# Kernel tuning notes

Measured on AMD Instinct MI355X. Metric: run time of the kernel, lower is better.

Reference implementation:

```python
import jax, jax.numpy as jnp
import numpy as np

NUM_CLS = 80
NUM_CONVS = 4
GROUPS = 32
STRIDES = [8, 16, 32, 64, 128]
SIZES = [32.0, 64.0, 128.0, 256.0, 512.0]
CLS_BIAS_INIT = -float(np.log((1 - 0.01) / 0.01))


def _conv(x, w, b):
    # NCHW 3x3 stride-1 same-pad conv
    y = jax.lax.conv_general_dilated(x, w, (1, 1), 'SAME',
                                     dimension_numbers=('NCHW', 'OIHW', 'NCHW'))
    return y + b[None, :, None, None]


def _group_norm(x, gamma, beta, eps=1e-5):
    B, C, H, W = x.shape
    xr = x.reshape(B, GROUPS, C // GROUPS, H, W)
    m = xr.mean(axis=(2, 3, 4), keepdims=True)
    v = xr.var(axis=(2, 3, 4), keepdims=True)
    xn = ((xr - m) / jnp.sqrt(v + eps)).reshape(B, C, H, W)
    return xn * gamma[None, :, None, None] + beta[None, :, None, None]


def _tower(x, ws, bs, gs, betas):
    # CGR block: Conv -> GroupNorm -> ReLU, repeated NUM_CONVS times
    for i in range(NUM_CONVS):
        x = jax.nn.relu(_group_norm(_conv(x, ws[i], bs[i]), gs[i], betas[i]))
    return x


def _build_anchors(h, w, stride, size):
    half = size / 2.0  # single scale=1, ratio=1 -> one square anchor per cell
    yv, xv = jnp.meshgrid(jnp.arange(h, dtype=jnp.float32),
                          jnp.arange(w, dtype=jnp.float32), indexing='ij')
    grid = jnp.stack([xv, yv, xv, yv], axis=-1)  # [h,w,4]
    delta = jnp.array([-half, -half, half, half], dtype=jnp.float32)
    return ((grid + 0.5) * stride + delta).reshape(-1, 4)  # [h*w,4]


def setup_inputs() -> dict:
    key = jax.random.key(0)
    ks = jax.random.split(key, 16)
    C = 256
    feats = {}
    hw = [80, 40, 20, 10, 5]
    for i, name in enumerate(['p3', 'p4', 'p5', 'p6', 'p7']):
        feats[name] = jax.random.normal(ks[i], (8, C, hw[i], hw[i]), dtype=jnp.float32)
    std = 0.01
    inp = dict(feats)
    # cls tower
    inp['cls_tw'] = jax.random.normal(ks[5], (NUM_CONVS, C, C, 3, 3), jnp.float32) * std
    inp['cls_tb'] = jnp.zeros((NUM_CONVS, C), jnp.float32)
    inp['cls_tg'] = jnp.ones((NUM_CONVS, C), jnp.float32)
    inp['cls_tbeta'] = jnp.zeros((NUM_CONVS, C), jnp.float32)
    # reg tower
    inp['reg_tw'] = jax.random.normal(ks[6], (NUM_CONVS, C, C, 3, 3), jnp.float32) * std
    inp['reg_tb'] = jnp.zeros((NUM_CONVS, C), jnp.float32)
    inp['reg_tg'] = jnp.ones((NUM_CONVS, C), jnp.float32)
    inp['reg_tbeta'] = jnp.zeros((NUM_CONVS, C), jnp.float32)
    # heads (num_anchors = 1)
    inp['cls_hw'] = jax.random.normal(ks[7], (NUM_CLS, C, 3, 3), jnp.float32) * std
    inp['cls_hb'] = jnp.full((NUM_CLS,), CLS_BIAS_INIT, jnp.float32)
    inp['reg_hw'] = jax.random.normal(ks[8], (4, C, 3, 3), jnp.float32) * std
    inp['reg_hb'] = jnp.zeros((4,), jnp.float32)
    inp['iou_hw'] = jax.random.normal(ks[9], (1, C, 3, 3), jnp.float32) * std
    inp['iou_hb'] = jnp.zeros((1,), jnp.float32)
    inp['scales'] = jnp.ones((5,), jnp.float32)
    return inp


def reference(p3, p4, p5, p6, p7,
              cls_tw, cls_tb, cls_tg, cls_tbeta,
              reg_tw, reg_tb, reg_tg, reg_tbeta,
              cls_hw, cls_hb, reg_hw, reg_hb, iou_hw, iou_hb, scales):
    feats = [p3, p4, p5, p6, p7]
    outs = []
    for j, x in enumerate(feats):
        B, _, H, W = x.shape
        ct = _tower(x, cls_tw, cls_tb, cls_tg, cls_tbeta)
        rt = _tower(x, reg_tw, reg_tb, reg_tg, reg_tbeta)
        # heads: permute to NHWC then flatten spatial (num_anchors=1)
        cls = _conv(ct, cls_hw, cls_hb).transpose(0, 2, 3, 1).reshape(B, -1, NUM_CLS)
        reg = _conv(rt, reg_hw, reg_hb).transpose(0, 2, 3, 1).reshape(B, -1, 4) * scales[j]
        iou = _conv(rt, iou_hw, iou_hb).transpose(0, 2, 3, 1).reshape(B, -1, 1)  # on_reg=True
        # decode boxes against anchors
        anchor = _build_anchors(H, W, STRIDES[j], SIZES[j])  # [HW,4]
        awh = anchor[:, 2:] - anchor[:, :2]
        actr = anchor[:, :2] + 0.5 * awh
        xy = reg[..., :2] * awh + actr
        wh = jnp.exp(reg[..., 2:]) * awh
        box = jnp.concatenate([xy - 0.5 * wh, xy + 0.5 * wh], axis=-1)
        outs.append(jnp.concatenate([box, iou, cls], axis=-1))
    return jnp.concatenate(outs, axis=1)  # [B, 8525, 85]
```

## Files before the change

kernel.cpp:

```cpp
#include <hip/hip_runtime.h>
#include <stdint.h>

typedef unsigned short u16;
typedef unsigned int u32;
typedef short short8 __attribute__((ext_vector_type(8)));
typedef float f32x4 __attribute__((ext_vector_type(4)));

#define GN_CHUNK 800
#define GN_MAXCH 8

struct LevelTab {
  int Hf[5], Wf[5], Hp[5], Wp[5], HW[5], M[5], mtcum[5], aoff[5];
  int gch[5];
  long xoffp[5], moff[5], ppcum[5], mcum[5];
  float asize[5], astride[5];
};

__device__ __forceinline__ u16 f2bf(float f) {
  u32 u = __float_as_uint(f);
  u = (u + 0x7fffu + ((u >> 16) & 1u)) >> 16;
  return (u16)u;
}
__device__ __forceinline__ float bflo(u32 v) { return __uint_as_float(v << 16); }
__device__ __forceinline__ float bfhi(u32 v) { return __uint_as_float(v & 0xffff0000u); }

__device__ __forceinline__ void gload16(const void* g, void* l) {
  __builtin_amdgcn_global_load_lds((__attribute__((address_space(1))) void*)(g),
                                   (__attribute__((address_space(3))) void*)(l),
                                   16, 0, 0);
}

__global__ __launch_bounds__(256) void prep_tower_w(const float* __restrict__ cls_tw,
                                                    const float* __restrict__ reg_tw,
                                                    u16* __restrict__ W2t) {
  long t = (long)blockIdx.x * 256 + threadIdx.x;
  const long total = 2L * 4 * 256 * 2304;
  if (t >= total) return;
  int ci = (int)(t & 255);
  long u = t >> 8;
  int j = (int)(u % 9); u /= 9;
  int co = (int)(u & 255); u >>= 8;
  int layer = (int)(u & 3);
  int tw = (int)(u >> 2);
  const float* src = tw ? reg_tw : cls_tw;
  float v = src[(((long)layer * 256 + co) * 256 + ci) * 9 + j];
  W2t[t] = f2bf(v);
}

__global__ __launch_bounds__(256) void prep_cls_w(const float* __restrict__ cls_hw,
                                                  u16* __restrict__ W2c) {
  long t = (long)blockIdx.x * 256 + threadIdx.x;
  if (t >= 128L * 2304) return;
  int ci = (int)(t & 255);
  long u = t >> 8;
  int j = (int)(u % 9);
  int co = (int)(u / 9);
  float v = (co < 80) ? cls_hw[(((long)co * 256 + ci) * 9 + j)] : 0.f;
  W2c[t] = f2bf(v);
}

__global__ __launch_bounds__(256) void prep_reg_w(const float* __restrict__ reg_hw,
                                                  const float* __restrict__ iou_hw,
                                                  u16* __restrict__ W2r) {
  long t = (long)blockIdx.x * 256 + threadIdx.x;
  if (t >= 5L * 2304) return;
  int ci = (int)(t & 255);
  long u = t >> 8;
  int j = (int)(u % 9);
  int o = (int)(u / 9);
  float v = (o < 4) ? reg_hw[(((long)o * 256 + ci) * 9 + j)] : iou_hw[(long)ci * 9 + j];
  W2r[t] = f2bf(v);
}

__global__ __launch_bounds__(256) void convert_in(const float* __restrict__ i0, const float* __restrict__ i1,
                                                  const float* __restrict__ i2, const float* __restrict__ i3,
                                                  const float* __restrict__ i4, u16* __restrict__ X0,
                                                  LevelTab lt) {
  long t = (long)blockIdx.x * 256 + threadIdx.x;
  if (t >= lt.ppcum[4] * 32) return;
  const int c8 = (int)(t & 31);
  long pp = t >> 5;
  int lvl = 0;
#pragma unroll
  for (int i = 0; i < 4; ++i) lvl += (pp >= lt.ppcum[i]);
  const long lp = pp - (lvl ? lt.ppcum[lvl - 1] : 0);
  const int Hp = lt.Hp[lvl], Wp = lt.Wp[lvl], Wf = lt.Wf[lvl], HW = lt.HW[lvl];
  const int HpWp = Hp * Wp;
  const int n = (int)(lp / HpWp);
  const int rem = (int)(lp - (long)n * HpWp);
  const int yp = rem / Wp, xp = rem - yp * Wp;
  u16* op = X0 + (lt.xoffp[lvl] + lp) * 256 + c8 * 8;
  if (yp == 0 || yp == Hp - 1 || xp == 0 || xp == Wp - 1) {
    *(uint4*)op = make_uint4(0u, 0u, 0u, 0u);
    return;
  }
  const float* src = lvl == 0 ? i0 : lvl == 1 ? i1 : lvl == 2 ? i2 : lvl == 3 ? i3 : i4;
  const int y = yp - 1, x = xp - 1;
  const long sb = ((long)n * 256 + c8 * 8) * HW + (long)y * Wf + x;
  u32 o4[4];
#pragma unroll
  for (int i = 0; i < 4; ++i) {
    float f0 = src[sb + (long)(2 * i) * HW];
    float f1 = src[sb + (long)(2 * i + 1) * HW];
    o4[i] = (u32)f2bf(f0) | ((u32)f2bf(f1) << 16);
  }
  *(uint4*)op = make_uint4(o4[0], o4[1], o4[2], o4[3]);
}

template <int MODE>
__global__ __launch_bounds__(256, 2) void conv_mfma(
    const u16* __restrict__ XpadA, const u16* __restrict__ XpadB,
    const u16* __restrict__ W2A, const u16* __restrict__ W2B,
    const float* __restrict__ biasA, const float* __restrict__ biasB,
    u16* __restrict__ OtmpA, u16* __restrict__ OtmpB,
    float* __restrict__ Oout, int NP, LevelTab lt) {
  __shared__ __align__(16) u16 sA[3][128 * 32];
  __shared__ __align__(16) u16 sB[3][128 * 32];

  const int nwg = gridDim.x;
  const int qq = nwg >> 3, rr = nwg & 7;
  const int xcd = blockIdx.x & 7, ib = blockIdx.x >> 3;
  const int sid = (xcd < rr ? xcd * (qq + 1) : rr * (qq + 1) + (xcd - rr) * qq) + ib;

  int path, tileId, nt;
  if (MODE == 0) {
    if (NP == 2) {
      const int half = nwg >> 1;
      path = (sid >= half) ? 1 : 0;
      const int inner = sid - path * half;
      tileId = inner >> 1;
      nt = inner & 1;
    } else {
      path = 0;
      tileId = sid >> 1;
      nt = sid & 1;
    }
  } else {
    path = 0;
    tileId = sid;
    nt = 0;
  }
  const u16* __restrict__ Xpad = path ? XpadB : XpadA;
  const u16* __restrict__ W2 = path ? W2B : W2A;
  const float* __restrict__ bias = path ? biasB : biasA;
  u16* __restrict__ Otmp = path ? OtmpB : OtmpA;

  int lvl = 0;
#pragma unroll
  for (int i = 0; i < 4; ++i) lvl += (tileId >= lt.mtcum[i]);
  const int mt = tileId - (lvl ? lt.mtcum[lvl - 1] : 0);
  const int Hp = lt.Hp[lvl], Wp = lt.Wp[lvl], Wf = lt.Wf[lvl];
  const int HW = lt.HW[lvl], M = lt.M[lvl];
  const long xbase = lt.xoffp[lvl] * 256;

  const int tid = threadIdx.x;
  const int w = tid >> 6, lane = tid & 63;
  const int rsub = lane >> 2;
  const int r0 = w * 16 + rsub;
  const int q2 = ((lane & 3) - ((lane >> 3) & 3)) & 3;

  long gA[2], gB[2];
#pragma unroll
  for (int i = 0; i < 2; ++i) {
    int ml = mt * 128 + r0 + i * 64;
    if (ml > M - 1) ml = M - 1;
    const int n = ml / HW;
    const int pr = ml - n * HW;
    const int y = pr / Wf;
    const int x = pr - y * Wf;
    gA[i] = xbase + ((long)((n * Hp + y) * Wp + x)) * 256 + q2 * 8;
    gB[i] = (long)(nt * 128 + r0 + i * 64) * 2304 + q2 * 8;
  }

  const int wm = w >> 1, wn = w & 1;
  const int lm = lane & 15;
  const int slot8 = ((((lane >> 4) + ((lane >> 1) & 3)) & 3) << 3);

  f32x4 acc[4][4];
#pragma unroll
  for (int a = 0; a < 4; ++a)
#pragma unroll
    for (int c = 0; c < 4; ++c) acc[a][c] = {0.f, 0.f, 0.f, 0.f};

  auto STAGE = [&](int kk, int buf) {
    const int j = kk >> 3;
    const int c0 = (kk & 7) << 5;
    const int jy = j / 3, jx = j - jy * 3;
    const long aK = ((long)(jy * Wp + jx)) * 256 + c0;
    const long bK = (long)kk << 5;
    gload16(Xpad + gA[0] + aK, sA[buf] + w * 512);
    gload16(Xpad + gA[1] + aK, sA[buf] + 2048 + w * 512);
    gload16(W2 + gB[0] + bK, sB[buf] + w * 512);
    gload16(W2 + gB[1] + bK, sB[buf] + 2048 + w * 512);
  };

  short8 a0[4], b0[4], a1[4], b1[4];
  auto FRAG0 = [&](int cur) {
    const u16* pa = sA[cur];
    const u16* pb = sB[cur];
#pragma unroll
    for (int mi = 0; mi < 4; ++mi)
      a0[mi] = *(const short8*)(pa + ((wm * 64 + mi * 16 + lm) << 5) + slot8);
#pragma unroll
    for (int ni = 0; ni < 4; ++ni)
      b0[ni] = *(const short8*)(pb + ((wn * 64 + ni * 16 + lm) << 5) + slot8);
  };
  auto FRAG1 = [&](int cur) {
    const u16* pa = sA[cur];
    const u16* pb = sB[cur];
#pragma unroll
    for (int mi = 0; mi < 4; ++mi)
      a1[mi] = *(const short8*)(pa + ((wm * 64 + mi * 16 + lm) << 5) + slot8);
#pragma unroll
    for (int ni = 0; ni < 4; ++ni)
      b1[ni] = *(const short8*)(pb + ((wn * 64 + ni * 16 + lm) << 5) + slot8);
  };
  auto MFMA0 = [&]() {
    __builtin_amdgcn_s_setprio(1);
#pragma unroll
    for (int mi = 0; mi < 4; ++mi)
#pragma unroll
      for (int ni = 0; ni < 4; ++ni)
        acc[mi][ni] = __builtin_amdgcn_mfma_f32_16x16x32_bf16(a0[mi], b0[ni], acc[mi][ni], 0, 0, 0);
    __builtin_amdgcn_s_setprio(0);
  };
  auto MFMA1 = [&]() {
    __builtin_amdgcn_s_setprio(1);
#pragma unroll
    for (int mi = 0; mi < 4; ++mi)
#pragma unroll
      for (int ni = 0; ni < 4; ++ni)
        acc[mi][ni] = __builtin_amdgcn_mfma_f32_16x16x32_bf16(a1[mi], b1[ni], acc[mi][ni], 0, 0, 0);
    __builtin_amdgcn_s_setprio(0);
  };

  STAGE(0, 0);
  STAGE(1, 1);
  asm volatile("s_waitcnt vmcnt(4)" ::: "memory");
  __builtin_amdgcn_s_barrier();
  FRAG0(0);
  STAGE(2, 2);

  int rd = 1;
  int st = 0;
  for (int kk = 0; kk < 68; kk += 2) {
    asm volatile("s_waitcnt vmcnt(4)" ::: "memory");
    __builtin_amdgcn_s_barrier();
    FRAG1(rd);
    rd = rd == 2 ? 0 : rd + 1;
    STAGE(kk + 3, st);
    st = st == 2 ? 0 : st + 1;
    MFMA0();
    asm volatile("s_waitcnt vmcnt(4)" ::: "memory");
    __builtin_amdgcn_s_barrier();
    FRAG0(rd);
    rd = rd == 2 ? 0 : rd + 1;
    STAGE(kk + 4, st);
    st = st == 2 ? 0 : st + 1;
    MFMA1();
  }
  asm volatile("s_waitcnt vmcnt(4)" ::: "memory");
  __builtin_amdgcn_s_barrier();
  FRAG1(rd);
  rd = rd == 2 ? 0 : rd + 1;
  STAGE(71, st);
  MFMA0();
  asm volatile("s_waitcnt vmcnt(4)" ::: "memory");
  __builtin_amdgcn_s_barrier();
  FRAG0(rd);
  rd = rd == 2 ? 0 : rd + 1;
  MFMA1();
  asm volatile("s_waitcnt vmcnt(0)" ::: "memory");
  __builtin_amdgcn_s_barrier();
  FRAG1(rd);
  MFMA0();
  MFMA1();

  const int mwb = mt * 128 + wm * 64;
  const int colb = nt * 128 + wn * 64;
  const int rq4 = (lane >> 4) << 2;
#pragma unroll
  for (int ni = 0; ni < 4; ++ni) {
    const int col = colb + ni * 16 + lm;
    if (MODE == 1 && col >= 80) continue;
    const float bv = bias[col];
#pragma unroll
    for (int mi = 0; mi < 4; ++mi) {
      const int rb = mwb + mi * 16 + rq4;
#pragma unroll
      for (int rg = 0; rg < 4; ++rg) {
        const int ml = rb + rg;
        if (ml < M) {
          const float v = acc[mi][ni][rg] + bv;
          if (MODE == 0) {
            Otmp[(lt.moff[lvl] + ml) * 256 + col] = f2bf(v);
          } else {
            const int nb = ml / HW;
            const int pr = ml - nb * HW;
            Oout[((long)nb * 8525 + lt.aoff[lvl] + pr) * 85 + 5 + col] = v;
          }
        }
      }
    }
  }
}

__global__ __launch_bounds__(256) void gn_part(const u16* __restrict__ tmpA,
                                               const u16* __restrict__ tmpB,
                                               float* __restrict__ part, int perPath,
                                               LevelTab lt) {
  const int bid = blockIdx.x;
  const int path = bid / perPath;
  int r = bid - path * perPath;
  int lvl = 0;
#pragma unroll
  for (int i = 0; i < 4; ++i) {
    const int c = 8 * lt.gch[i];
    if (r >= c) { r -= c; lvl = i + 1; } else break;
  }
  const int b = r / lt.gch[lvl];
  const int chunk = r - b * lt.gch[lvl];
  const u16* __restrict__ tmp = path ? tmpB : tmpA;
  const int HW = lt.HW[lvl];
  const int start = chunk * GN_CHUNK;
  const int end = (start + GN_CHUNK < HW) ? start + GN_CHUNK : HW;

  const int tid = threadIdx.x;
  const int c8 = tid & 31, po = tid >> 5;
  const long base = (lt.moff[lvl] + (long)b * HW) * 256 + c8 * 8;
  float s = 0.f, ss = 0.f;
  for (int p = start + po; p < end; p += 8) {
    const uint4 r4 = *(const uint4*)(tmp + base + (long)p * 256);
    const u32 u[4] = {r4.x, r4.y, r4.z, r4.w};
#pragma unroll
    for (int i = 0; i < 4; ++i) {
      float f0 = bflo(u[i]), f1 = bfhi(u[i]);
      s += f0 + f1;
      ss += f0 * f0 + f1 * f1;
    }
  }
  s += __shfl_down(s, 32);
  ss += __shfl_down(ss, 32);
  __shared__ float rs[4][32], rss[4][32];
  const int w = tid >> 6, lane = tid & 63;
  if (lane < 32) { rs[w][lane] = s; rss[w][lane] = ss; }
  __syncthreads();
  if (tid < 32) {
    const float S = rs[0][tid] + rs[1][tid] + rs[2][tid] + rs[3][tid];
    const float SS = rss[0][tid] + rss[1][tid] + rss[2][tid] + rss[3][tid];
    const long slot = ((long)((path * 1280 + lvl * 256 + b * 32 + tid) * GN_MAXCH + chunk)) * 2;
    part[slot] = S;
    part[slot + 1] = SS;
  }
}

__global__ __launch_bounds__(256) void gn_final(const float* __restrict__ part,
                                                float* __restrict__ stats, LevelTab lt) {
  const int idx = blockIdx.x * 256 + threadIdx.x;
  if (idx >= 2 * 1280) return;
  const int lb = idx % 1280;
  const int lvl = lb >> 8;
  const int nch = lt.gch[lvl];
  float s = 0.f, ss = 0.f;
  const long sbase = (long)idx * GN_MAXCH * 2;
  for (int c = 0; c < nch; ++c) {
    s += part[sbase + c * 2];
    ss += part[sbase + c * 2 + 1];
  }
  const float inv = 1.f / (float)(lt.HW[lvl] * 8);
  const float mean = s * inv;
  const float var = ss * inv - mean * mean;
  stats[idx * 2 + 0] = mean;
  stats[idx * 2 + 1] = rsqrtf(var + 1e-5f);
}

__global__ __launch_bounds__(256) void gn_apply(const u16* __restrict__ tmpA,
                                                const u16* __restrict__ tmpB,
                                                const float* __restrict__ stats,
                                                const float* __restrict__ gammaA,
                                                const float* __restrict__ betaA,
                                                const float* __restrict__ gammaB,
                                                const float* __restrict__ betaB,
                                                u16* __restrict__ poutA, u16* __restrict__ poutB,
                                                int ppBlocks, LevelTab lt) {
  const int path = blockIdx.x / ppBlocks;
  const int xb = blockIdx.x - path * ppBlocks;
  const u16* __restrict__ tmp = path ? tmpB : tmpA;
  const float* __restrict__ gamma = path ? gammaB : gammaA;
  const float* __restrict__ beta = path ? betaB : betaA;
  u16* __restrict__ pout = path ? poutB : poutA;

  long t = (long)xb * 256 + threadIdx.x;
  if (t >= lt.ppcum[4] * 32) return;
  const int c8 = (int)(t & 31);
  long pp = t >> 5;
  int lvl = 0;
#pragma unroll
  for (int i = 0; i < 4; ++i) lvl += (pp >= lt.ppcum[i]);
  const long lp = pp - (lvl ? lt.ppcum[lvl - 1] : 0);
  const int Hp = lt.Hp[lvl], Wp = lt.Wp[lvl], Wf = lt.Wf[lvl], HW = lt.HW[lvl];
  const int HpWp = Hp * Wp;
  const int n = (int)(lp / HpWp);
  const int rem = (int)(lp - (long)n * HpWp);
  const int yp = rem / Wp, xp = rem - yp * Wp;
  u16* op = pout + (lt.xoffp[lvl] + lp) * 256 + c8 * 8;
  if (yp == 0 || yp == Hp - 1 || xp == 0 || xp == Wp - 1) {
    *(uint4*)op = make_uint4(0u, 0u, 0u, 0u);
    return;
  }
  const long m = lt.moff[lvl] + (long)n * HW + (long)(yp - 1) * Wf + (xp - 1);
  const uint4 r = *(const uint4*)(tmp + m * 256 + c8 * 8);
  const int sidx = (path * 1280 + lvl * 256 + n * 32 + c8) * 2;
  const float mean = stats[sidx], rstd = stats[sidx + 1];
  const u32 u[4] = {r.x, r.y, r.z, r.w};
  u32 o4[4];
#pragma unroll
  for (int i = 0; i < 4; ++i) {
    const int c = c8 * 8 + i * 2;
    float f0 = (bflo(u[i]) - mean) * rstd * gamma[c] + beta[c];
    float f1 = (bfhi(u[i]) - mean) * rstd * gamma[c + 1] + beta[c + 1];
    f0 = fmaxf(f0, 0.f);
    f1 = fmaxf(f1, 0.f);
    o4[i] = (u32)f2bf(f0) | ((u32)f2bf(f1) << 16);
  }
  *(uint4*)op = make_uint4(o4[0], o4[1], o4[2], o4[3]);
}

__global__ __launch_bounds__(256) void regiou_decode(const u16* __restrict__ Xp,
                                                     const u16* __restrict__ W2r,
                                                     const float* __restrict__ reg_hb,
                                                     const float* __restrict__ iou_hb,
                                                     const float* __restrict__ scales,
                                                     float* __restrict__ out, LevelTab lt) {
  const long gt = (long)blockIdx.x * 256 + threadIdx.x;
  const int gw = (int)(gt >> 6);
  const int lane = threadIdx.x & 63;
  if (gw >= (int)lt.mcum[4]) return;
  int lvl = 0;
#pragma unroll
  for (int i = 0; i < 4; ++i) lvl += (gw >= (int)lt.mcum[i]);
  const int m = gw - (int)(lvl ? lt.mcum[lvl - 1] : 0);
  const int HW = lt.HW[lvl], Wf = lt.Wf[lvl], Hp = lt.Hp[lvl], Wp = lt.Wp[lvl];
  const int b = m / HW, pr = m - b * HW;
  const int y = pr / Wf, x = pr - y * Wf;
  const long base = (lt.xoffp[lvl] + (long)(b * Hp + y) * Wp + x) * 256 + lane * 4;
  float acc[5] = {0.f, 0.f, 0.f, 0.f, 0.f};
#pragma unroll
  for (int j = 0; j < 9; ++j) {
    const int jy = j / 3, jx = j - jy * 3;
    const uint2 ar = *(const uint2*)(Xp + base + ((long)(jy * Wp + jx)) * 256);
    const float x0 = bflo(ar.x), x1 = bfhi(ar.x), x2 = bflo(ar.y), x3 = bfhi(ar.y);
#pragma unroll
    for (int o = 0; o < 5; ++o) {
      const uint2 wr = *(const uint2*)(W2r + o * 2304 + j * 256 + lane * 4);
      acc[o] += x0 * bflo(wr.x) + x1 * bfhi(wr.x) + x2 * bflo(wr.y) + x3 * bfhi(wr.y);
    }
  }
#pragma unroll
  for (int o = 0; o < 5; ++o)
#pragma unroll
    for (int d = 32; d; d >>= 1) acc[o] += __shfl_down(acc[o], d);
  if (lane == 0) {
    const float sc = scales[lvl];
    const float r0 = (acc[0] + reg_hb[0]) * sc;
    const float r1 = (acc[1] + reg_hb[1]) * sc;
    const float r2 = (acc[2] + reg_hb[2]) * sc;
    const float r3 = (acc[3] + reg_hb[3]) * sc;
    const float iou = acc[4] + iou_hb[0];
    const float st = lt.astride[lvl], sz = lt.asize[lvl];
    const float cx = (x + 0.5f) * st, cy = (y + 0.5f) * st;
    const float xx = r0 * sz + cx, yy = r1 * sz + cy;
    const float ww = expf(r2) * sz, hh = expf(r3) * sz;
    float* o = out + ((long)b * 8525 + lt.aoff[lvl] + pr) * 85;
    o[0] = xx - 0.5f * ww;
    o[1] = yy - 0.5f * hh;
    o[2] = xx + 0.5f * ww;
    o[3] = yy + 0.5f * hh;
    o[4] = iou;
  }
}

extern "C" void kernel_launch(void* const* d_in, const int* in_sizes, int n_in, void* d_out,
                              int out_size, void* d_ws, size_t ws_size, hipStream_t stream) {
  const float* feats[5];
  for (int i = 0; i < 5; ++i) feats[i] = (const float*)d_in[i];
  const float* cls_tw = (const float*)d_in[5];
  const float* cls_tb = (const float*)d_in[6];
  const float* cls_tg = (const float*)d_in[7];
  const float* cls_tbeta = (const float*)d_in[8];
  const float* reg_tw = (const float*)d_in[9];
  const float* reg_tb = (const float*)d_in[10];
  const float* reg_tg = (const float*)d_in[11];
  const float* reg_tbeta = (const float*)d_in[12];
  const float* cls_hw = (const float*)d_in[13];
  const float* cls_hb = (const float*)d_in[14];
  const float* reg_hw = (const float*)d_in[15];
  const float* reg_hb = (const float*)d_in[16];
  const float* iou_hw = (const float*)d_in[17];
  const float* iou_hb = (const float*)d_in[18];
  const float* scales = (const float*)d_in[19];
  float* out = (float*)d_out;

  LevelTab lt;
  const int Hs[5] = {80, 40, 20, 10, 5};
  const float sizes[5] = {32.f, 64.f, 128.f, 256.f, 512.f};
  const float strides[5] = {8.f, 16.f, 32.f, 64.f, 128.f};
  long ppc = 0, mc = 0;
  int mtc = 0, ao = 0, chTot = 0;
  for (int i = 0; i < 5; ++i) {
    const int H = Hs[i];
    lt.Hf[i] = H; lt.Wf[i] = H; lt.Hp[i] = H + 2; lt.Wp[i] = H + 2;
    lt.HW[i] = H * H; lt.M[i] = 8 * H * H;
    lt.gch[i] = (H * H + GN_CHUNK - 1) / GN_CHUNK;
    lt.xoffp[i] = ppc; lt.moff[i] = mc; lt.aoff[i] = ao;
    ppc += 8L * (H + 2) * (H + 2);
    mc += lt.M[i];
    mtc += (lt.M[i] + 127) / 128;
    lt.ppcum[i] = ppc; lt.mcum[i] = mc; lt.mtcum[i] = mtc;
    ao += H * H;
    chTot += lt.gch[i];
    lt.asize[i] = sizes[i]; lt.astride[i] = strides[i];
  }
  const int perPath = 8 * chTot;

  char* ws = (char*)d_ws;
  size_t off = 0;
  auto take = [&](size_t bytes) {
    off = (off + 255) & ~(size_t)255;
    char* p = ws + off;
    off += bytes;
    return p;
  };
  auto alg = [](size_t v) { return (v + 255) & ~(size_t)255; };
  const size_t sizeX = alg((size_t)ppc * 512);
  const size_t sizeT = alg((size_t)mc * 512);
  const size_t wTsz = alg((size_t)2 * 4 * 256 * 2304 * 2);
  const size_t wCsz = alg((size_t)128 * 2304 * 2);
  const size_t wRsz = alg((size_t)5 * 2304 * 2);
  const size_t pSz = alg((size_t)2 * 1280 * GN_MAXCH * 2 * 4);
  const size_t sSz = alg((size_t)2 * 1280 * 2 * 4);
  const size_t needMerged = 4 * sizeX + 2 * sizeT + wTsz + wCsz + wRsz + pSz + sSz + 4096;
  const bool MERGED = (ws_size >= needMerged);

  const int ppBlocks = (int)((ppc * 32 + 255) / 256);

  if (MERGED) {
    u16* X0 = (u16*)take(sizeX);
    u16* C1 = (u16*)take(sizeX);
    u16* R0 = (u16*)take(sizeX);
    u16* R1 = (u16*)take(sizeX);
    u16* tmpA = (u16*)take(sizeT);
    u16* tmpB = (u16*)take(sizeT);
    u16* W2t = (u16*)take(wTsz);
    u16* W2c = (u16*)take(wCsz);
    u16* W2r = (u16*)take(wRsz);
    float* part = (float*)take(pSz);
    float* stats = (float*)take(sSz);

    prep_tower_w<<<(int)((2L * 4 * 256 * 2304 + 255) / 256), 256, 0, stream>>>(cls_tw, reg_tw, W2t);
    prep_cls_w<<<(int)((128L * 2304 + 255) / 256), 256, 0, stream>>>(cls_hw, W2c);
    prep_reg_w<<<(int)((5L * 2304 + 255) / 256), 256, 0, stream>>>(reg_hw, iou_hw, W2r);
    convert_in<<<ppBlocks, 256, 0, stream>>>(feats[0], feats[1], feats[2], feats[3], feats[4],
                                             X0, lt);

    u16* wrA[4] = {X0, C1, X0, C1};
    u16* wrB[4] = {R0, R1, R0, R1};
    const u16* curA = X0;
    const u16* curB = X0;
    for (int layer = 0; layer < 4; ++layer) {
      const u16* w2A = W2t + (size_t)(0 * 4 + layer) * 256 * 2304;
      const u16* w2B = W2t + (size_t)(1 * 4 + layer) * 256 * 2304;
      conv_mfma<0><<<mtc * 2 * 2, 256, 0, stream>>>(curA, curB, w2A, w2B,
                                                    cls_tb + layer * 256, reg_tb + layer * 256,
                                                    tmpA, tmpB, nullptr, 2, lt);
      gn_part<<<2 * perPath, 256, 0, stream>>>(tmpA, tmpB, part, perPath, lt);
      gn_final<<<10, 256, 0, stream>>>(part, stats, lt);
      gn_apply<<<2 * ppBlocks, 256, 0, stream>>>(tmpA, tmpB, stats,
                                                 cls_tg + layer * 256, cls_tbeta + layer * 256,
                                                 reg_tg + layer * 256, reg_tbeta + layer * 256,
                                                 wrA[layer], wrB[layer], ppBlocks, lt);
      curA = wrA[layer];
      curB = wrB[layer];
    }
    conv_mfma<1><<<mtc, 256, 0, stream>>>(curA, curA, W2c, W2c, cls_hb, cls_hb,
                                          nullptr, nullptr, out, 1, lt);
    regiou_decode<<<(int)((mc * 64 + 255) / 256), 256, 0, stream>>>(curB, W2r, reg_hb, iou_hb,
                                                                    scales, out, lt);
  } else {
    u16* X0 = (u16*)take(sizeX);
    u16* padA = (u16*)take(sizeX);
    u16* padB = (u16*)take(sizeX);
    u16* tmp = (u16*)take(sizeT);
    u16* W2t = (u16*)take(wTsz);
    u16* W2c = (u16*)take(wCsz);
    u16* W2r = (u16*)take(wRsz);
    float* part = (float*)take(pSz);
    float* stats = (float*)take(sSz);

    prep_tower_w<<<(int)((2L * 4 * 256 * 2304 + 255) / 256), 256, 0, stream>>>(cls_tw, reg_tw, W2t);
    prep_cls_w<<<(int)((128L * 2304 + 255) / 256), 256, 0, stream>>>(cls_hw, W2c);
    prep_reg_w<<<(int)((5L * 2304 + 255) / 256), 256, 0, stream>>>(reg_hw, iou_hw, W2r);
    convert_in<<<ppBlocks, 256, 0, stream>>>(feats[0], feats[1], feats[2], feats[3], feats[4],
                                             X0, lt);

    u16* pads[2] = {padA, padB};
    for (int tw = 0; tw < 2; ++tw) {
      const float* tb = tw ? reg_tb : cls_tb;
      const float* tg = tw ? reg_tg : cls_tg;
      const float* tbe = tw ? reg_tbeta : cls_tbeta;
      const u16* cur = X0;
      for (int layer = 0; layer < 4; ++layer) {
        const u16* w2 = W2t + (size_t)(tw * 4 + layer) * 256 * 2304;
        conv_mfma<0><<<mtc * 2, 256, 0, stream>>>(cur, cur, w2, w2, tb + layer * 256,
                                                  tb + layer * 256, tmp, tmp, nullptr, 1, lt);
        gn_part<<<perPath, 256, 0, stream>>>(tmp, tmp, part, perPath, lt);
        gn_final<<<10, 256, 0, stream>>>(part, stats, lt);
        u16* nxt = pads[layer & 1];
        gn_apply<<<ppBlocks, 256, 0, stream>>>(tmp, tmp, stats, tg + layer * 256,
                                               tbe + layer * 256, tg + layer * 256,
                                               tbe + layer * 256, nxt, nxt, ppBlocks, lt);
        cur = nxt;
      }
      if (tw == 0) {
        conv_mfma<1><<<mtc, 256, 0, stream>>>(cur, cur, W2c, W2c, cls_hb, cls_hb,
                                              nullptr, nullptr, out, 1, lt);
      } else {
        regiou_decode<<<(int)((mc * 64 + 255) / 256), 256, 0, stream>>>(cur, W2r, reg_hb, iou_hb,
                                                                        scales, out, lt);
      }
    }
  }
}
```

Measured before the change: 1.346 ms.

## Replace tower conv with 256x256-tile 512-thread MFMA kernel

Adds a conv256 kernel that computes a 256-pixel by 256-channel output tile per workgroup with 8 waves, double-buffered LDS staging via global_load_lds, and 16x16x32 bf16 MFMA. Each tile now covers all output channels, so input pixels are loaded once per tile instead of once per 128-channel half, which raises operand reuse per LDS load. The cost is fewer, larger workgroups with 128 KB of LDS and one block per CU, which lowers occupancy and load balance on the small pyramid levels.

```diff
diff --git a/kernel.cpp b/kernel.cpp
--- a/kernel.cpp
+++ b/kernel.cpp
@@ -10,7 +10,7 @@
 #define GN_MAXCH 8
 
 struct LevelTab {
-  int Hf[5], Wf[5], Hp[5], Wp[5], HW[5], M[5], mtcum[5], aoff[5];
+  int Hf[5], Wf[5], Hp[5], Wp[5], HW[5], M[5], mtcum[5], mt256[5], aoff[5];
   int gch[5];
   long xoffp[5], moff[5], ppcum[5], mcum[5];
   float asize[5], astride[5];
@@ -105,6 +105,143 @@
     o4[i] = (u32)f2bf(f0) | ((u32)f2bf(f1) << 16);
   }
   *(uint4*)op = make_uint4(o4[0], o4[1], o4[2], o4[3]);
+}
+
+__global__ __launch_bounds__(512, 1) void conv256(
+    const u16* __restrict__ XpadA, const u16* __restrict__ XpadB,
+    const u16* __restrict__ W2A, const u16* __restrict__ W2B,
+    const float* __restrict__ biasA, const float* __restrict__ biasB,
+    u16* __restrict__ OtmpA, u16* __restrict__ OtmpB, int NP, LevelTab lt) {
+  __shared__ __align__(16) u16 lds[2][4][256 * 32];
+
+  const int nwg = gridDim.x;
+  const int qq = nwg >> 3, rr = nwg & 7;
+  const int xcd = blockIdx.x & 7, ib = blockIdx.x >> 3;
+  const int sid = (xcd < rr ? xcd * (qq + 1) : rr * (qq + 1) + (xcd - rr) * qq) + ib;
+  int path, tileId;
+  if (NP == 2) {
+    const int half = nwg >> 1;
+    path = (sid >= half) ? 1 : 0;
+    tileId = sid - path * half;
+  } else {
+    path = 0;
+    tileId = sid;
+  }
+  const u16* __restrict__ Xpad = path ? XpadB : XpadA;
+  const u16* __restrict__ W2 = path ? W2B : W2A;
+  const float* __restrict__ bias = path ? biasB : biasA;
+  u16* __restrict__ Otmp = path ? OtmpB : OtmpA;
+
+  int lvl = 0;
+#pragma unroll
+  for (int i = 0; i < 4; ++i) lvl += (tileId >= lt.mt256[i]);
+  const int mt = tileId - (lvl ? lt.mt256[lvl - 1] : 0);
+  const int Hp = lt.Hp[lvl], Wp = lt.Wp[lvl], Wf = lt.Wf[lvl];
+  const int HW = lt.HW[lvl], M = lt.M[lvl];
+  const long xbase = lt.xoffp[lvl] * 256;
+
+  const int tid = threadIdx.x;
+  const int w = tid >> 6, lane = tid & 63;
+  const int wm = w >> 2, wn = w & 3;
+  const int lm = lane & 15, hi = lane >> 4;
+
+  long pixA[2], rowB[2];
+#pragma unroll
+  for (int j = 0; j < 2; ++j) {
+    const int rl = (w * 2 + j) * 16 + (lane >> 2);
+    int ml = mt * 256 + rl;
+    if (ml > M - 1) ml = M - 1;
+    const int n = ml / HW;
+    const int pr = ml - n * HW;
+    const int y = pr / Wf;
+    const int x = pr - y * Wf;
+    pixA[j] = xbase + ((long)((n * Hp + y) * Wp + x)) * 256 + (lane & 3) * 8;
+    rowB[j] = (long)rl * 2304 + (lane & 3) * 8;
+  }
+
+  f32x4 acc[8][4];
+#pragma unroll
+  for (int a = 0; a < 8; ++a)
+#pragma unroll
+    for (int c = 0; c < 4; ++c) acc[a][c] = {0.f, 0.f, 0.f, 0.f};
+
+  auto STAGE_CH = [&](int kt, int ch) {
+    const int tap = kt >> 2;
+    const int jy = tap / 3, jx = tap - jy * 3;
+    const long c0 = (long)((kt & 3) * 64 + (ch >> 1) * 32);
+    u16* dst = &lds[kt & 1][ch][0] + w * 1024;
+    if ((ch & 1) == 0) {
+      const long aoff = ((long)(jy * Wp + jx)) * 256 + c0;
+      gload16(Xpad + pixA[0] + aoff, dst);
+      gload16(Xpad + pixA[1] + aoff, dst + 512);
+    } else {
+      const long boff = (long)tap * 256 + c0;
+      gload16(W2 + rowB[0] + boff, dst);
+      gload16(W2 + rowB[1] + boff, dst + 512);
+    }
+  };
+
+  STAGE_CH(0, 0);
+  STAGE_CH(0, 1);
+  STAGE_CH(0, 2);
+  STAGE_CH(0, 3);
+  asm volatile("s_waitcnt vmcnt(4)" ::: "memory");
+  __builtin_amdgcn_s_barrier();
+
+  short8 af[4], bfv[4];
+  const int NT = 36;
+  for (int kt = 0; kt < NT; ++kt) {
+    const int buf = kt & 1;
+#pragma unroll
+    for (int q = 0; q < 4; ++q) {
+      const int ks = q >> 1, mh = q & 1;
+      const u16* pa = &lds[buf][ks * 2][0];
+#pragma unroll
+      for (int mi2 = 0; mi2 < 4; ++mi2)
+        af[mi2] = *(const short8*)(pa + ((wm * 128 + (mh * 4 + mi2) * 16 + lm) * 32 + hi * 8));
+      if (mh == 0) {
+        const u16* pb = &lds[buf][ks * 2 + 1][0];
+#pragma unroll
+        for (int ni = 0; ni < 4; ++ni)
+          bfv[ni] = *(const short8*)(pb + ((wn * 64 + ni * 16 + lm) * 32 + hi * 8));
+      }
+      if (kt + 1 < NT) STAGE_CH(kt + 1, q);
+      if (mh == 1) {
+        if (kt + 1 < NT)
+          asm volatile("s_waitcnt vmcnt(4)" ::: "memory");
+        else
+          asm volatile("s_waitcnt vmcnt(0)" ::: "memory");
+      }
+      __builtin_amdgcn_s_barrier();
+      __builtin_amdgcn_s_setprio(1);
+#pragma unroll
+      for (int mi2 = 0; mi2 < 4; ++mi2)
+#pragma unroll
+        for (int ni = 0; ni < 4; ++ni)
+          acc[mh * 4 + mi2][ni] =
+              __builtin_amdgcn_mfma_f32_16x16x32_bf16(af[mi2], bfv[ni], acc[mh * 4 + mi2][ni], 0, 0, 0);
+      __builtin_amdgcn_s_setprio(0);
+      __builtin_amdgcn_s_barrier();
+    }
+  }
+
+  const int mwb = mt * 256 + wm * 128;
+  const int colb = wn * 64;
+  const int rq4 = hi << 2;
+#pragma unroll
+  for (int ni = 0; ni < 4; ++ni) {
+    const int col = colb + ni * 16 + lm;
+    const float bv = bias[col];
+#pragma unroll
+    for (int mi = 0; mi < 8; ++mi) {
+      const int rb = mwb + mi * 16 + rq4;
+#pragma unroll
+      for (int rg = 0; rg < 4; ++rg) {
+        const int ml = rb + rg;
+        if (ml < M) Otmp[(lt.moff[lvl] + ml) * 256 + col] = f2bf(acc[mi][ni][rg] + bv);
+      }
+    }
+  }
 }
 
 template <int MODE>
@@ -506,7 +643,7 @@
   const float sizes[5] = {32.f, 64.f, 128.f, 256.f, 512.f};
   const float strides[5] = {8.f, 16.f, 32.f, 64.f, 128.f};
   long ppc = 0, mc = 0;
-  int mtc = 0, ao = 0, chTot = 0;
+  int mtc = 0, mt256c = 0, ao = 0, chTot = 0;
   for (int i = 0; i < 5; ++i) {
     const int H = Hs[i];
     lt.Hf[i] = H; lt.Wf[i] = H; lt.Hp[i] = H + 2; lt.Wp[i] = H + 2;
@@ -516,7 +653,8 @@
     ppc += 8L * (H + 2) * (H + 2);
     mc += lt.M[i];
     mtc += (lt.M[i] + 127) / 128;
-    lt.ppcum[i] = ppc; lt.mcum[i] = mc; lt.mtcum[i] = mtc;
+    mt256c += (lt.M[i] + 255) / 256;
+    lt.ppcum[i] = ppc; lt.mcum[i] = mc; lt.mtcum[i] = mtc; lt.mt256[i] = mt256c;
     ao += H * H;
     chTot += lt.gch[i];
     lt.asize[i] = sizes[i]; lt.astride[i] = strides[i];
@@ -570,9 +708,9 @@
     for (int layer = 0; layer < 4; ++layer) {
       const u16* w2A = W2t + (size_t)(0 * 4 + layer) * 256 * 2304;
       const u16* w2B = W2t + (size_t)(1 * 4 + layer) * 256 * 2304;
-      conv_mfma<0><<<mtc * 2 * 2, 256, 0, stream>>>(curA, curB, w2A, w2B,
-                                                    cls_tb + layer * 256, reg_tb + layer * 256,
-                                                    tmpA, tmpB, nullptr, 2, lt);
+      conv256<<<mt256c * 2, 512, 0, stream>>>(curA, curB, w2A, w2B,
+                                              cls_tb + layer * 256, reg_tb + layer * 256,
+                                              tmpA, tmpB, 2, lt);
       gn_part<<<2 * perPath, 256, 0, stream>>>(tmpA, tmpB, part, perPath, lt);
       gn_final<<<10, 256, 0, stream>>>(part, stats, lt);
       gn_apply<<<2 * ppBlocks, 256, 0, stream>>>(tmpA, tmpB, stats,
@@ -611,8 +749,8 @@
       const u16* cur = X0;
       for (int layer = 0; layer < 4; ++layer) {
         const u16* w2 = W2t + (size_t)(tw * 4 + layer) * 256 * 2304;
-        conv_mfma<0><<<mtc * 2, 256, 0, stream>>>(cur, cur, w2, w2, tb + layer * 256,
-                                                  tb + layer * 256, tmp, tmp, nullptr, 1, lt);
+        conv256<<<mt256c, 512, 0, stream>>>(cur, cur, w2, w2, tb + layer * 256,
+                                            tb + layer * 256, tmp, tmp, 1, lt);
         gn_part<<<perPath, 256, 0, stream>>>(tmp, tmp, part, perPath, lt);
         gn_final<<<10, 256, 0, stream>>>(part, stats, lt);
         u16* nxt = pads[layer & 1];
```

After: 1.463 ms. 8.8% more time.
